# Kernel optimization log

Measured on AMD Instinct MI355X. Metric: run time of the kernel, lower is better.

Reference implementation:

```python
import jax, jax.numpy as jnp
import numpy as np

EPS = 1e-7
MAX_TANGENT_NORM = 1.5
SCALE = 16.0 / 8.0  # alpha / rank


def _exp_map_zero(vs, K, max_norm):
    # vs: [..., n] spatial tangent at origin (time component is 0).
    # Returns (x0, xs): Lorentz point time/spatial parts, <x,x>_L = -1/K.
    sqrtK = jnp.sqrt(K)
    n = jnp.linalg.norm(vs, axis=-1, keepdims=True)
    nc = jnp.minimum(n, max_norm)                       # clamp tangent norm (TB-PAG)
    vs_c = vs * (nc / jnp.maximum(n, EPS))
    t = sqrtK * nc
    x0 = jnp.cosh(t) / sqrtK
    xs = jnp.sinh(t) / (sqrtK * jnp.maximum(nc, EPS)) * vs_c
    return x0, xs


def _log_map_zero_spatial(x0, xs, K):
    # Inverse of exp at origin; returns spatial part of tangent vector.
    sqrtK = jnp.sqrt(K)
    d = jnp.arccosh(jnp.maximum(sqrtK * x0, 1.0 + EPS)) / sqrtK  # geodesic distance
    ns = jnp.linalg.norm(xs, axis=-1, keepdims=True)
    return d * xs / jnp.maximum(ns, EPS)


def setup_inputs() -> dict:
    key = jax.random.key(0)
    k1, k2, k3, k4, k5 = jax.random.split(key, 5)
    Bsz, S, D, R = 4, 2048, 4096, 8
    x = jax.random.normal(k1, (Bsz, S, D), dtype=jnp.float32)
    W = jax.random.normal(k2, (D, D), dtype=jnp.float32) * (1.0 / np.sqrt(D))
    b = jax.random.normal(k3, (D,), dtype=jnp.float32) * 0.01
    A = jax.random.normal(k4, (D, R), dtype=jnp.float32) * 0.01
    B = jax.random.normal(k5, (R, D), dtype=jnp.float32) * 0.01
    log_K = jnp.zeros((), dtype=jnp.float32)  # K = 1.0
    return {"x": x, "W": W, "b": b, "A": A, "B": B, "log_K": log_K}


def reference(x, W, b, A, B, log_K):
    K = jnp.clip(jnp.exp(log_K), 1e-4, 10.0)
    # frozen Euclidean base: z = x @ W^T + b
    z_base = jnp.einsum('bsd,od->bso', x, W) + b
    # project Euclidean hidden state onto H^n: exp_map_zero([0, x])
    x0, xs = _exp_map_zero(x, K, MAX_TANGENT_NORM)
    # LLR: tangent vector at origin, rank-r bottleneck, back to manifold
    v = _log_map_zero_spatial(x0, xs, K)            # [b,s,d]
    v_adapted = (v @ A) @ B                          # rank-8 bottleneck
    y0, ys = _exp_map_zero(v_adapted, K, MAX_TANGENT_NORM)
    # project back to Euclidean (spatial slice of log map)
    delta = _log_map_zero_spatial(y0, ys, K)
    return z_base + delta * SCALE
```

## Files before the change

kernel.cpp:

```cpp
#include <hip/hip_runtime.h>
#include <hip/hip_bf16.h>


#define DD 4096
#define MR 8192
#define BM 256
#define BN 256
#define BK 64

typedef float f32x4 __attribute__((ext_vector_type(4)));
typedef __bf16 bf16x8 __attribute__((ext_vector_type(8)));

#define GLOAD_LDS16(gptr, lptr)                                                        \
  __builtin_amdgcn_global_load_lds((const __attribute__((address_space(1))) void*)(gptr), \
                                   (__attribute__((address_space(3))) void*)(lptr), 16, 0, 0)

__device__ __forceinline__ __bf16 f2bf(float f) { return (__bf16)f; }

__global__ __launch_bounds__(256) void k_prep(const float* __restrict__ x,
                                              const float* __restrict__ W,
                                              const float* __restrict__ A,
                                              const float* __restrict__ Bm,
                                              __bf16* __restrict__ Xb,
                                              __bf16* __restrict__ Wb,
                                              float* __restrict__ U,
                                              float* __restrict__ G) {
  int bid = blockIdx.x;
  int t = threadIdx.x;
  int lane = t & 63, wid = t >> 6;

  if (bid == 0) {
    float g[64];
#pragma unroll
    for (int i = 0; i < 64; ++i) g[i] = 0.f;
    for (int d = t; d < DD; d += 256) {
      float br[8];
#pragma unroll
      for (int r = 0; r < 8; ++r) br[r] = Bm[r * DD + d];
#pragma unroll
      for (int r = 0; r < 8; ++r)
#pragma unroll
        for (int s = 0; s < 8; ++s) g[r * 8 + s] += br[r] * br[s];
    }
    __shared__ float gs[4][64];
#pragma unroll
    for (int i = 0; i < 64; ++i) {
      float v = g[i];
      for (int off = 32; off >= 1; off >>= 1) v += __shfl_down(v, off, 64);
      if (lane == 0) gs[wid][i] = v;
    }
    __syncthreads();
    if (t < 64) G[t] = gs[0][t] + gs[1][t] + gs[2][t] + gs[3][t];
  } else if (bid <= 2048) {
    int r0 = (bid - 1) * 4;
    const float* xr0 = x + (size_t)r0 * DD;
    __bf16* xb0 = Xb + (size_t)r0 * DD;
    float nsq[4] = {0.f, 0.f, 0.f, 0.f};
    float p[4][8] = {};
#pragma unroll
    for (int i = 0; i < 16; ++i) {
      int d = t + 256 * i;
      f32x4 a0 = *reinterpret_cast<const f32x4*>(A + (size_t)d * 8);
      f32x4 a1 = *reinterpret_cast<const f32x4*>(A + (size_t)d * 8 + 4);
#pragma unroll
      for (int r = 0; r < 4; ++r) {
        float xv = xr0[(size_t)r * DD + d];
        xb0[(size_t)r * DD + d] = f2bf(xv);
        nsq[r] += xv * xv;
        p[r][0] += xv * a0[0]; p[r][1] += xv * a0[1];
        p[r][2] += xv * a0[2]; p[r][3] += xv * a0[3];
        p[r][4] += xv * a1[0]; p[r][5] += xv * a1[1];
        p[r][6] += xv * a1[2]; p[r][7] += xv * a1[3];
      }
    }
    for (int off = 32; off >= 1; off >>= 1) {
#pragma unroll
      for (int r = 0; r < 4; ++r) {
        nsq[r] += __shfl_down(nsq[r], off, 64);
#pragma unroll
        for (int q = 0; q < 8; ++q) p[r][q] += __shfl_down(p[r][q], off, 64);
      }
    }
    __shared__ float red[4][36];
    if (lane == 0) {
#pragma unroll
      for (int r = 0; r < 4; ++r) {
        red[wid][r * 9] = nsq[r];
#pragma unroll
        for (int q = 0; q < 8; ++q) red[wid][r * 9 + 1 + q] = p[r][q];
      }
    }
    __syncthreads();
    if (t < 4) {
      float ns = red[0][t * 9] + red[1][t * 9] + red[2][t * 9] + red[3][t * 9];
      float u[8];
#pragma unroll
      for (int q = 0; q < 8; ++q)
        u[q] = red[0][t * 9 + 1 + q] + red[1][t * 9 + 1 + q] +
               red[2][t * 9 + 1 + q] + red[3][t * 9 + 1 + q];
      float n = sqrtf(ns);
      float s1 = fminf(n, 1.5f) / fmaxf(n, 1e-7f);
#pragma unroll
      for (int q = 0; q < 8; ++q) U[(size_t)(r0 + t) * 8 + q] = s1 * u[q];
    }
  } else {
    int i = (bid - 2049) * 256 + t;
    const f32x4* s = reinterpret_cast<const f32x4*>(W) + (size_t)i * 2;
    f32x4 v0 = s[0], v1 = s[1];
    bf16x8 o;
    o[0] = f2bf(v0[0]); o[1] = f2bf(v0[1]); o[2] = f2bf(v0[2]); o[3] = f2bf(v0[3]);
    o[4] = f2bf(v1[0]); o[5] = f2bf(v1[1]); o[6] = f2bf(v1[2]); o[7] = f2bf(v1[3]);
    reinterpret_cast<bf16x8*>(Wb)[i] = o;
  }
}

__global__ __launch_bounds__(512, 2) void k_gemm(const __bf16* __restrict__ Xb,
                                                 const __bf16* __restrict__ Wb,
                                                 const float* __restrict__ bias,
                                                 const float* __restrict__ U,
                                                 const float* __restrict__ G,
                                                 const float* __restrict__ Bm,
                                                 float* __restrict__ out) {
  __shared__ union {
    char raw[131072];
    struct { float cs[256][8]; float bs2[8][256]; } epi;
  } sm;
  char* smc = sm.raw;

  const int nwg = (MR / BM) * (DD / BN);
  int wg = ((int)blockIdx.x % 8) * (nwg / 8) + (int)blockIdx.x / 8;
  int tm = wg / (DD / BN);
  int tn = wg % (DD / BN);
  int row0 = tm * BM, col0 = tn * BN;

  int t = threadIdx.x;
  int lane = t & 63, wid = t >> 6;
  int wm = wid >> 2, wn = wid & 3;
  int fr = lane & 15;
  int hi = lane >> 4;
  int sw = (fr >> 1) & 3;

  f32x4 acc[8][4] = {};
  bf16x8 aA[4], aB[4], bA[4], bB[4];

  auto STAGE = [&](const __bf16* mat, int rowbase, int tau, int ks, int ldsOff) {
    int j = (t & 3) ^ ((t >> 3) & 3);
    int kk = ((tau & 63) << 6) + (ks << 5) + (j << 3);
    const __bf16* src = mat + (size_t)(rowbase + (t >> 2)) * DD + kk;
    char* dst = smc + ldsOff + t * 16;
    GLOAD_LDS16(src, dst);
    GLOAD_LDS16(src + (size_t)128 * DD, dst + 8192);
  };

#define LDA(dst, buf, ks, mbase)                                                \
  _Pragma("unroll") for (int j = 0; j < 4; ++j) dst[j] =                        \
      *reinterpret_cast<const bf16x8*>(smc + (buf)*65536 + 16384 + (ks)*32768 + \
                                       (wm * 128 + ((mbase) + j) * 16 + fr) * 64 + \
                                       ((hi ^ sw) << 4));
#define LDB(dst, buf, ks)                                                       \
  _Pragma("unroll") for (int j = 0; j < 4; ++j) dst[j] =                        \
      *reinterpret_cast<const bf16x8*>(smc + (buf)*65536 + (ks)*32768 +         \
                                       (wn * 64 + j * 16 + fr) * 64 +           \
                                       ((hi ^ sw) << 4));
#define MMQ(aset, bset, mbase)                                                  \
  __builtin_amdgcn_s_setprio(1);                                                \
  _Pragma("unroll") for (int j = 0; j < 4; ++j)                                 \
      _Pragma("unroll") for (int n = 0; n < 4; ++n)                             \
          acc[(mbase) + j][n] = __builtin_amdgcn_mfma_f32_16x16x32_bf16(        \
              aset[j], bset[n], acc[(mbase) + j][n], 0, 0, 0);                  \
  __builtin_amdgcn_s_setprio(0);
#define BAR() __builtin_amdgcn_s_barrier()
#define VM6() asm volatile("s_waitcnt vmcnt(6)" ::: "memory")
#define SGB_PIN(nreads)                                      \
  __builtin_amdgcn_sched_group_barrier(0x100, (nreads), 0);  \
  __builtin_amdgcn_sched_group_barrier(0x8, 16, 0)

  STAGE(Wb, col0, 0, 0, 0);
  STAGE(Xb, row0, 0, 0, 16384);
  STAGE(Wb, col0, 0, 1, 32768);
  STAGE(Xb, row0, 0, 1, 49152);
  asm volatile("s_waitcnt vmcnt(4)" ::: "memory");
  STAGE(Wb, col0, 1, 0, 65536 + 0);
  STAGE(Xb, row0, 1, 0, 65536 + 16384);
  STAGE(Wb, col0, 1, 1, 65536 + 32768);
  VM6();
  BAR();
  LDA(aA, 0, 0, 0);
  LDB(bA, 0, 0);

  for (int i = 0; i < DD / BK / 2; ++i) {
    int T = 2 * i;
    STAGE(Xb, row0, T + 1, 1, 65536 + 49152);
    BAR();
    LDA(aB, 0, 0, 4);
    MMQ(aA, bA, 0);
    SGB_PIN(4);
    BAR();
    STAGE(Wb, col0, T + 2, 0, 0);
    BAR();
    LDA(aA, 0, 1, 0);
    LDB(bB, 0, 1);
    MMQ(aB, bA, 4);
    SGB_PIN(8);
    BAR();
    STAGE(Xb, row0, T + 2, 0, 16384);
    BAR();
    LDA(aB, 0, 1, 4);
    MMQ(aA, bB, 0);
    SGB_PIN(4);
    BAR();
    STAGE(Wb, col0, T + 2, 1, 32768);
    BAR();
    VM6();
    LDA(aA, 1, 0, 0);
    LDB(bA, 1, 0);
    MMQ(aB, bB, 4);
    SGB_PIN(8);
    BAR();
    STAGE(Xb, row0, T + 2, 1, 49152);
    BAR();
    LDA(aB, 1, 0, 4);
    MMQ(aA, bA, 0);
    SGB_PIN(4);
    BAR();
    STAGE(Wb, col0, T + 3, 0, 65536 + 0);
    BAR();
    LDA(aA, 1, 1, 0);
    LDB(bB, 1, 1);
    MMQ(aB, bA, 4);
    SGB_PIN(8);
    BAR();
    STAGE(Xb, row0, T + 3, 0, 65536 + 16384);
    BAR();
    LDA(aB, 1, 1, 4);
    MMQ(aA, bB, 0);
    SGB_PIN(4);
    BAR();
    STAGE(Wb, col0, T + 3, 1, 65536 + 32768);
    BAR();
    VM6();
    LDA(aA, 0, 0, 0);
    LDB(bA, 0, 0);
    MMQ(aB, bB, 4);
    SGB_PIN(8);
    BAR();
  }

  asm volatile("s_waitcnt vmcnt(0)" ::: "memory");
  __syncthreads();
  {
    int rr = t >> 6, cc = (t & 63) * 4;
    *reinterpret_cast<f32x4*>(&sm.epi.bs2[rr][cc]) =
        *reinterpret_cast<const f32x4*>(Bm + (size_t)rr * DD + col0 + cc);
  }
  if (t < 256) {
    f32x4 u0 = *reinterpret_cast<const f32x4*>(U + (size_t)(row0 + t) * 8);
    f32x4 u1 = *reinterpret_cast<const f32x4*>(U + (size_t)(row0 + t) * 8 + 4);
    float u[8] = {u0[0], u0[1], u0[2], u0[3], u1[0], u1[1], u1[2], u1[3]};
    float n2sq = 0.f;
#pragma unroll
    for (int r = 0; r < 8; ++r) {
      float s = 0.f;
#pragma unroll
      for (int q = 0; q < 8; ++q) s += G[r * 8 + q] * u[q];
      n2sq += u[r] * s;
    }
    float n2 = sqrtf(fmaxf(n2sq, 0.f));
    float sc2 = 2.0f * fminf(n2, 1.5f) / fmaxf(n2, 1e-7f);
#pragma unroll
    for (int r = 0; r < 8; ++r) sm.epi.cs[t][r] = sc2 * u[r];
  }
  __syncthreads();

  int colb = col0 + wn * 64 + fr;
  float biasv[4], bcol[4][8];
#pragma unroll
  for (int n = 0; n < 4; ++n) {
    biasv[n] = bias[colb + n * 16];
#pragma unroll
    for (int r = 0; r < 8; ++r) bcol[n][r] = sm.epi.bs2[r][wn * 64 + fr + n * 16];
  }
#pragma unroll
  for (int m = 0; m < 8; ++m) {
#pragma unroll
    for (int j = 0; j < 4; ++j) {
      int rl = wm * 128 + m * 16 + hi * 4 + j;
      float c0 = sm.epi.cs[rl][0], c1 = sm.epi.cs[rl][1], c2 = sm.epi.cs[rl][2],
            c3 = sm.epi.cs[rl][3], c4 = sm.epi.cs[rl][4], c5 = sm.epi.cs[rl][5],
            c6 = sm.epi.cs[rl][6], c7 = sm.epi.cs[rl][7];
      float* orow = out + (size_t)(row0 + rl) * DD + colb;
#pragma unroll
      for (int n = 0; n < 4; ++n) {
        float delta = c0 * bcol[n][0] + c1 * bcol[n][1] + c2 * bcol[n][2] +
                      c3 * bcol[n][3] + c4 * bcol[n][4] + c5 * bcol[n][5] +
                      c6 * bcol[n][6] + c7 * bcol[n][7];
        orow[n * 16] = acc[m][n][j] + biasv[n] + delta;
      }
    }
  }
}

extern "C" void kernel_launch(void* const* d_in, const int* in_sizes, int n_in,
                              void* d_out, int out_size, void* d_ws, size_t ws_size,
                              hipStream_t stream) {
  const float* x = (const float*)d_in[0];
  const float* W = (const float*)d_in[1];
  const float* b = (const float*)d_in[2];
  const float* A = (const float*)d_in[3];
  const float* Bm = (const float*)d_in[4];
  float* out = (float*)d_out;

  char* ws = (char*)d_ws;
  __bf16* Xb = (__bf16*)ws;
  __bf16* Wb = (__bf16*)(ws + (size_t)64 * 1024 * 1024);
  float* U = (float*)(ws + (size_t)96 * 1024 * 1024);
  float* G = (float*)(ws + (size_t)96 * 1024 * 1024 + 256 * 1024);

  k_prep<<<1 + 2048 + 8192, 256, 0, stream>>>(x, W, A, Bm, Xb, Wb, U, G);
  k_gemm<<<(MR / BM) * (DD / BN), 512, 0, stream>>>(Xb, Wb, b, U, G, Bm, out);
}
```

Before: 303.4 us.

## Simplify GEMM main loop to full-tile LDS loads then 32-MFMA bursts

Replaces the fine-grained 8-phase ping-pong schedule, which interleaved half-tile LDS fragment loads with 16-MFMA groups and pinned instruction order with sched_group_barriers, with a simpler 4-phase loop. Each phase loads all 8 A and 4 B fragments, issues two global-to-LDS stages, waits for LDS reads to finish, and then runs 32 MFMAs. This cuts barrier count and scheduling constraints. In exchange, LDS read latency is no longer hidden behind MFMAs, and more fragment registers are live at once.

```diff
diff --git a/kernel.cpp b/kernel.cpp
--- a/kernel.cpp
+++ b/kernel.cpp
@@ -141,7 +141,7 @@
   int sw = (fr >> 1) & 3;
 
   f32x4 acc[8][4] = {};
-  bf16x8 aA[4], aB[4], bA[4], bB[4];
+  bf16x8 aF[8], bF[4];
 
   auto STAGE = [&](const __bf16* mat, int rowbase, int tau, int ks, int ldsOff) {
     int j = (t & 3) ^ ((t >> 3) & 3);
@@ -152,98 +152,63 @@
     GLOAD_LDS16(src + (size_t)128 * DD, dst + 8192);
   };
 
-#define LDA(dst, buf, ks, mbase)                                                \
-  _Pragma("unroll") for (int j = 0; j < 4; ++j) dst[j] =                        \
+#define LDA8(buf, ks)                                                           \
+  _Pragma("unroll") for (int j = 0; j < 8; ++j) aF[j] =                         \
       *reinterpret_cast<const bf16x8*>(smc + (buf)*65536 + 16384 + (ks)*32768 + \
-                                       (wm * 128 + ((mbase) + j) * 16 + fr) * 64 + \
+                                       (wm * 128 + j * 16 + fr) * 64 +          \
                                        ((hi ^ sw) << 4));
-#define LDB(dst, buf, ks)                                                       \
-  _Pragma("unroll") for (int j = 0; j < 4; ++j) dst[j] =                        \
+#define LDB4(buf, ks)                                                           \
+  _Pragma("unroll") for (int j = 0; j < 4; ++j) bF[j] =                         \
       *reinterpret_cast<const bf16x8*>(smc + (buf)*65536 + (ks)*32768 +         \
                                        (wn * 64 + j * 16 + fr) * 64 +           \
                                        ((hi ^ sw) << 4));
-#define MMQ(aset, bset, mbase)                                                  \
+#define MM32()                                                                  \
   __builtin_amdgcn_s_setprio(1);                                                \
-  _Pragma("unroll") for (int j = 0; j < 4; ++j)                                 \
+  _Pragma("unroll") for (int m = 0; m < 8; ++m)                                 \
       _Pragma("unroll") for (int n = 0; n < 4; ++n)                             \
-          acc[(mbase) + j][n] = __builtin_amdgcn_mfma_f32_16x16x32_bf16(        \
-              aset[j], bset[n], acc[(mbase) + j][n], 0, 0, 0);                  \
+          acc[m][n] = __builtin_amdgcn_mfma_f32_16x16x32_bf16(                  \
+              aF[m], bF[n], acc[m][n], 0, 0, 0);                                \
   __builtin_amdgcn_s_setprio(0);
 #define BAR() __builtin_amdgcn_s_barrier()
-#define VM6() asm volatile("s_waitcnt vmcnt(6)" ::: "memory")
-#define SGB_PIN(nreads)                                      \
-  __builtin_amdgcn_sched_group_barrier(0x100, (nreads), 0);  \
-  __builtin_amdgcn_sched_group_barrier(0x8, 16, 0)
+#define LGKM0() asm volatile("s_waitcnt lgkmcnt(0)" ::: "memory")
+#define SB0() __builtin_amdgcn_sched_barrier(0)
+#define VM8() asm volatile("s_waitcnt vmcnt(8)" ::: "memory")
 
   STAGE(Wb, col0, 0, 0, 0);
   STAGE(Xb, row0, 0, 0, 16384);
   STAGE(Wb, col0, 0, 1, 32768);
   STAGE(Xb, row0, 0, 1, 49152);
-  asm volatile("s_waitcnt vmcnt(4)" ::: "memory");
-  STAGE(Wb, col0, 1, 0, 65536 + 0);
+  STAGE(Wb, col0, 1, 0, 65536);
   STAGE(Xb, row0, 1, 0, 65536 + 16384);
-  STAGE(Wb, col0, 1, 1, 65536 + 32768);
-  VM6();
+  VM8();
   BAR();
-  LDA(aA, 0, 0, 0);
-  LDB(bA, 0, 0);
-
-  for (int i = 0; i < DD / BK / 2; ++i) {
+
+  for (int i = 0; i < 32; ++i) {
     int T = 2 * i;
+    LDA8(0, 0); LDB4(0, 0);
+    STAGE(Wb, col0, T + 1, 1, 65536 + 32768);
     STAGE(Xb, row0, T + 1, 1, 65536 + 49152);
-    BAR();
-    LDA(aB, 0, 0, 4);
-    MMQ(aA, bA, 0);
-    SGB_PIN(4);
-    BAR();
+    BAR(); LGKM0(); SB0();
+    MM32();
+    VM8(); BAR();
+    LDA8(0, 1); LDB4(0, 1);
     STAGE(Wb, col0, T + 2, 0, 0);
-    BAR();
-    LDA(aA, 0, 1, 0);
-    LDB(bB, 0, 1);
-    MMQ(aB, bA, 4);
-    SGB_PIN(8);
-    BAR();
     STAGE(Xb, row0, T + 2, 0, 16384);
-    BAR();
-    LDA(aB, 0, 1, 4);
-    MMQ(aA, bB, 0);
-    SGB_PIN(4);
-    BAR();
+    BAR(); LGKM0(); SB0();
+    MM32();
+    VM8(); BAR();
+    LDA8(1, 0); LDB4(1, 0);
     STAGE(Wb, col0, T + 2, 1, 32768);
-    BAR();
-    VM6();
-    LDA(aA, 1, 0, 0);
-    LDB(bA, 1, 0);
-    MMQ(aB, bB, 4);
-    SGB_PIN(8);
-    BAR();
     STAGE(Xb, row0, T + 2, 1, 49152);
-    BAR();
-    LDA(aB, 1, 0, 4);
-    MMQ(aA, bA, 0);
-    SGB_PIN(4);
-    BAR();
-    STAGE(Wb, col0, T + 3, 0, 65536 + 0);
-    BAR();
-    LDA(aA, 1, 1, 0);
-    LDB(bB, 1, 1);
-    MMQ(aB, bA, 4);
-    SGB_PIN(8);
-    BAR();
+    BAR(); LGKM0(); SB0();
+    MM32();
+    VM8(); BAR();
+    LDA8(1, 1); LDB4(1, 1);
+    STAGE(Wb, col0, T + 3, 0, 65536);
     STAGE(Xb, row0, T + 3, 0, 65536 + 16384);
-    BAR();
-    LDA(aB, 1, 1, 4);
-    MMQ(aA, bB, 0);
-    SGB_PIN(4);
-    BAR();
-    STAGE(Wb, col0, T + 3, 1, 65536 + 32768);
-    BAR();
-    VM6();
-    LDA(aA, 0, 0, 0);
-    LDB(bA, 0, 0);
-    MMQ(aB, bB, 4);
-    SGB_PIN(8);
-    BAR();
+    BAR(); LGKM0(); SB0();
+    MM32();
+    VM8(); BAR();
   }
 
   asm volatile("s_waitcnt vmcnt(0)" ::: "memory");
```

Result: slower. 310.7 us (+2.4%).

## Drop register double-buffering of MFMA fragments and sched group barriers

Applied to the files above, without the earlier changes.

Replaces the ping-pong A/B fragment registers, where the next LDS reads overlap the current MFMA block, with a single fragment set loaded right before each MFMA block. The sched_group_barrier pinning that interleaved ds_reads with MFMAs is removed. This lowers register pressure but serializes the LDS reads with the matrix ops, so LDS latency is no longer hidden within a wave. Correctness looks preserved, since fragments are read after the barriers that follow the stage waits.

```diff
diff --git a/kernel.cpp b/kernel.cpp
--- a/kernel.cpp
+++ b/kernel.cpp
@@ -141,7 +141,7 @@
   int sw = (fr >> 1) & 3;
 
   f32x4 acc[8][4] = {};
-  bf16x8 aA[4], aB[4], bA[4], bB[4];
+  bf16x8 aF[4], bF[4];
 
   auto STAGE = [&](const __bf16* mat, int rowbase, int tau, int ks, int ldsOff) {
     int j = (t & 3) ^ ((t >> 3) & 3);
@@ -152,28 +152,25 @@
     GLOAD_LDS16(src + (size_t)128 * DD, dst + 8192);
   };
 
-#define LDA(dst, buf, ks, mbase)                                                \
-  _Pragma("unroll") for (int j = 0; j < 4; ++j) dst[j] =                        \
+#define LDA(buf, ks, mbase)                                                     \
+  _Pragma("unroll") for (int j = 0; j < 4; ++j) aF[j] =                         \
       *reinterpret_cast<const bf16x8*>(smc + (buf)*65536 + 16384 + (ks)*32768 + \
                                        (wm * 128 + ((mbase) + j) * 16 + fr) * 64 + \
                                        ((hi ^ sw) << 4));
-#define LDB(dst, buf, ks)                                                       \
-  _Pragma("unroll") for (int j = 0; j < 4; ++j) dst[j] =                        \
+#define LDB(buf, ks)                                                            \
+  _Pragma("unroll") for (int j = 0; j < 4; ++j) bF[j] =                         \
       *reinterpret_cast<const bf16x8*>(smc + (buf)*65536 + (ks)*32768 +         \
                                        (wn * 64 + j * 16 + fr) * 64 +           \
                                        ((hi ^ sw) << 4));
-#define MMQ(aset, bset, mbase)                                                  \
+#define MMQ(mbase)                                                              \
   __builtin_amdgcn_s_setprio(1);                                                \
   _Pragma("unroll") for (int j = 0; j < 4; ++j)                                 \
       _Pragma("unroll") for (int n = 0; n < 4; ++n)                             \
           acc[(mbase) + j][n] = __builtin_amdgcn_mfma_f32_16x16x32_bf16(        \
-              aset[j], bset[n], acc[(mbase) + j][n], 0, 0, 0);                  \
+              aF[j], bF[n], acc[(mbase) + j][n], 0, 0, 0);                      \
   __builtin_amdgcn_s_setprio(0);
 #define BAR() __builtin_amdgcn_s_barrier()
 #define VM6() asm volatile("s_waitcnt vmcnt(6)" ::: "memory")
-#define SGB_PIN(nreads)                                      \
-  __builtin_amdgcn_sched_group_barrier(0x100, (nreads), 0);  \
-  __builtin_amdgcn_sched_group_barrier(0x8, 16, 0)
 
   STAGE(Wb, col0, 0, 0, 0);
   STAGE(Xb, row0, 0, 0, 16384);
@@ -185,64 +182,50 @@
   STAGE(Wb, col0, 1, 1, 65536 + 32768);
   VM6();
   BAR();
-  LDA(aA, 0, 0, 0);
-  LDB(bA, 0, 0);
-
-  for (int i = 0; i < DD / BK / 2; ++i) {
+
+  for (int i = 0; i < 32; ++i) {
     int T = 2 * i;
+    LDA(0, 0, 0); LDB(0, 0);
     STAGE(Xb, row0, T + 1, 1, 65536 + 49152);
     BAR();
-    LDA(aB, 0, 0, 4);
-    MMQ(aA, bA, 0);
-    SGB_PIN(4);
-    BAR();
+    MMQ(0);
+    BAR();
+    LDA(0, 0, 4);
     STAGE(Wb, col0, T + 2, 0, 0);
     BAR();
-    LDA(aA, 0, 1, 0);
-    LDB(bB, 0, 1);
-    MMQ(aB, bA, 4);
-    SGB_PIN(8);
-    BAR();
+    MMQ(4);
+    BAR();
+    LDA(0, 1, 0); LDB(0, 1);
     STAGE(Xb, row0, T + 2, 0, 16384);
     BAR();
-    LDA(aB, 0, 1, 4);
-    MMQ(aA, bB, 0);
-    SGB_PIN(4);
-    BAR();
+    MMQ(0);
+    BAR();
+    LDA(0, 1, 4);
     STAGE(Wb, col0, T + 2, 1, 32768);
     BAR();
+    MMQ(4);
     VM6();
-    LDA(aA, 1, 0, 0);
-    LDB(bA, 1, 0);
-    MMQ(aB, bB, 4);
-    SGB_PIN(8);
-    BAR();
+    BAR();
+    LDA(1, 0, 0); LDB(1, 0);
     STAGE(Xb, row0, T + 2, 1, 49152);
     BAR();
-    LDA(aB, 1, 0, 4);
-    MMQ(aA, bA, 0);
-    SGB_PIN(4);
-    BAR();
+    MMQ(0);
+    BAR();
+    LDA(1, 0, 4);
     STAGE(Wb, col0, T + 3, 0, 65536 + 0);
     BAR();
-    LDA(aA, 1, 1, 0);
-    LDB(bB, 1, 1);
-    MMQ(aB, bA, 4);
-    SGB_PIN(8);
-    BAR();
+    MMQ(4);
+    BAR();
+    LDA(1, 1, 0); LDB(1, 1);
     STAGE(Xb, row0, T + 3, 0, 65536 + 16384);
     BAR();
-    LDA(aB, 1, 1, 4);
-    MMQ(aA, bB, 0);
-    SGB_PIN(4);
-    BAR();
+    MMQ(0);
+    BAR();
+    LDA(1, 1, 4);
     STAGE(Wb, col0, T + 3, 1, 65536 + 32768);
     BAR();
+    MMQ(4);
     VM6();
-    LDA(aA, 0, 0, 0);
-    LDB(bA, 0, 0);
-    MMQ(aB, bB, 4);
-    SGB_PIN(8);
     BAR();
   }
 
```

New measurement: 306.9 us. Within noise of the previous version (+1.2%).
